# Kernel optimization log

Hardware: AMD Instinct MI355X
Metric: run time of the kernel (lower is better)

Reference implementation:

```python
import jax, jax.numpy as jnp
import numpy as np

N_NODES = 50000
N_EDGES = 800000
IN_C, HID_C, OUT_C = 96, 64, 40
ALPHA = 0.2
K = 2
NEG_SLOPE = 0.01  # F.leaky_relu default


def setup_inputs() -> dict:
    key = jax.random.key(0)
    k_x, k_e, k_w0, k_b0, k_w4, k_b4 = jax.random.split(key, 6)
    x = jax.random.normal(k_x, (N_NODES, IN_C), dtype=jnp.float32)
    edge_index = jax.random.randint(k_e, (2, N_EDGES), 0, N_NODES, dtype=jnp.int64)
    # SGConv linear layers (torch.nn.Linear layout: [out, in])
    W0 = jax.random.normal(k_w0, (HID_C, IN_C), dtype=jnp.float32) / np.sqrt(IN_C)
    b0 = jax.random.normal(k_b0, (HID_C,), dtype=jnp.float32) * 0.01
    W4 = jax.random.normal(k_w4, (OUT_C, HID_C), dtype=jnp.float32) / np.sqrt(HID_C)
    b4 = jax.random.normal(k_b4, (OUT_C,), dtype=jnp.float32) * 0.01
    return {"x": x, "edge_index": edge_index, "W0": W0, "b0": b0, "W4": W4, "b4": b4}


def reference(x, edge_index, W0, b0, W4, b4):
    # GCN normalization with self-loops (shared by SGConv and APPNP in PyG):
    # A_hat = A + I, prop(h) = D^{-1/2} A_hat D^{-1/2} h
    n = x.shape[0]
    loops = jnp.arange(n, dtype=edge_index.dtype)
    src = jnp.concatenate([edge_index[0], loops])
    dst = jnp.concatenate([edge_index[1], loops])
    deg = jax.ops.segment_sum(jnp.ones_like(dst, dtype=x.dtype), dst, num_segments=n)
    dinv = jnp.where(deg > 0, jax.lax.rsqrt(deg), 0.0)
    norm = dinv[src] * dinv[dst]  # [E + N]

    def prop(h):
        # gather -> scale -> scatter-add  (irregular memory-bound core op)
        return jax.ops.segment_sum(norm[:, None] * h[src], dst, num_segments=n)

    def sg_prop(h):  # SGConv: K propagation steps, then linear
        for _ in range(K):
            h = prop(h)
        return h

    def appnp(h0):  # APPNP: z_{k+1} = (1-alpha) * prop(z_k) + alpha * h0
        z = h0
        for _ in range(K):
            z = (1.0 - ALPHA) * prop(z) + ALPHA * h0
        return z

    h = sg_prop(x) @ W0.T + b0          # conv0 (SGConv)
    # dropout is identity in eval mode (training=False)
    h = jax.nn.leaky_relu(appnp(h), NEG_SLOPE)   # conv1
    h = jax.nn.leaky_relu(appnp(h), NEG_SLOPE)   # conv2
    h = jax.nn.leaky_relu(appnp(h), NEG_SLOPE)   # conv3
    h = sg_prop(h) @ W4.T + b4          # conv4 (SGConv)
    return jax.nn.log_softmax(h, axis=1)
```

## Files before the change

### kernel.cpp

```cpp
#include <hip/hip_runtime.h>
#include <hip/hip_fp16.h>
#include <math.h>

#define N_NODES 50000
#define N_EDGES 800000
#define IN_C 96
#define HID_C 64
#define OUT_C 40
#define ALPHA 0.2f
#define NEG_SLOPE 0.01f

typedef _Float16 f16x8 __attribute__((ext_vector_type(8)));
typedef float f32x4 __attribute__((ext_vector_type(4)));

__device__ __forceinline__ int edge_at(const void* ei, int is64, long long pos) {
    return is64 ? (int)((const long long*)ei)[pos] : ((const int*)ei)[pos];
}

__global__ void zero_detect_k(int* deg, int n, const unsigned int* ei, int* flag) {
    int i = blockIdx.x * blockDim.x + threadIdx.x;
    if (i < n) deg[i] = 0;
    if (i == 0) {
        int is64 = 1;
        for (int j = 1; j < 16; j += 2)
            if (ei[j] != 0u) is64 = 0;
        *flag = is64;
    }
}

__global__ void deg_hist_k(const void* ei, const int* flag, int* deg, int E) {
    int e = blockIdx.x * blockDim.x + threadIdx.x;
    if (e < E) {
        int d = edge_at(ei, *flag, (long long)E + e);
        atomicAdd(&deg[d], 1);
    }
}

__global__ void scan_p1_k(const int* __restrict__ deg, int* __restrict__ part, int n) {
    __shared__ int sm[256];
    int t = threadIdx.x, i = blockIdx.x * 256 + t;
    int v = (i < n) ? deg[i] : 0;
    sm[t] = v;
    __syncthreads();
    for (int off = 1; off < 256; off <<= 1) {
        int u = (t >= off) ? sm[t - off] : 0;
        __syncthreads();
        sm[t] += u;
        __syncthreads();
    }
    if (t == 255) part[blockIdx.x] = sm[255];
}

__global__ void scan_p2_k(int* part, int nb, int* rowptr, int n) {
    __shared__ int sm[256];
    int t = threadIdx.x;
    int v = (t < nb) ? part[t] : 0;
    sm[t] = v;
    __syncthreads();
    for (int off = 1; off < 256; off <<= 1) {
        int u = (t >= off) ? sm[t - off] : 0;
        __syncthreads();
        sm[t] += u;
        __syncthreads();
    }
    if (t < nb) part[t] = sm[t] - v;
    if (t == 255) rowptr[n] = sm[255];
}

__global__ void scan_p3_k(const int* __restrict__ deg, const int* __restrict__ part,
                          int* __restrict__ rowptr, int* __restrict__ cursor,
                          float* __restrict__ dinv, int n) {
    __shared__ int sm[256];
    int t = threadIdx.x, i = blockIdx.x * 256 + t;
    int v = (i < n) ? deg[i] : 0;
    sm[t] = v;
    __syncthreads();
    for (int off = 1; off < 256; off <<= 1) {
        int u = (t >= off) ? sm[t - off] : 0;
        __syncthreads();
        sm[t] += u;
        __syncthreads();
    }
    if (i < n) {
        int excl = sm[t] - v + part[blockIdx.x];
        rowptr[i] = excl;
        cursor[i] = excl;
        dinv[i] = rsqrtf((float)v + 1.0f);
    }
}

__global__ void bhist_k(const int* __restrict__ deg, int* __restrict__ bcnt, int n) {
    __shared__ int h[64];
    int t = threadIdx.x, i = blockIdx.x * 256 + t;
    if (t < 64) h[t] = 0;
    __syncthreads();
    if (i < n) {
        int d = deg[i]; if (d > 63) d = 63;
        atomicAdd(&h[63 - d], 1);
    }
    __syncthreads();
    if (t < 64) bcnt[blockIdx.x * 64 + t] = h[t];
}

__global__ void bscanA_k(const int* __restrict__ bcnt, int* __restrict__ bbase,
                         int* __restrict__ tot, int nb) {
    __shared__ int sm[256];
    int b = blockIdx.x;
    int t = threadIdx.x;
    int v = (t < nb) ? bcnt[t * 64 + b] : 0;
    sm[t] = v;
    __syncthreads();
    for (int off = 1; off < 256; off <<= 1) {
        int u = (t >= off) ? sm[t - off] : 0;
        __syncthreads();
        sm[t] += u;
        __syncthreads();
    }
    if (t < nb) bbase[t * 64 + b] = sm[t] - v;
    if (t == 255) tot[b] = sm[255];
}

__global__ void bscanB_k(const int* __restrict__ tot, int* __restrict__ bstart) {
    __shared__ int sm[64];
    int t = threadIdx.x;
    int v = tot[t];
    sm[t] = v;
    __syncthreads();
    for (int off = 1; off < 64; off <<= 1) {
        int u = (t >= off) ? sm[t - off] : 0;
        __syncthreads();
        sm[t] += u;
        __syncthreads();
    }
    bstart[t] = sm[t] - v;
}

__global__ void perm_k(const int* __restrict__ deg, const int* __restrict__ bbase,
                       const int* __restrict__ bstart, int* __restrict__ perm, int n) {
    __shared__ int h[64];
    int t = threadIdx.x, i = blockIdx.x * 256 + t;
    if (t < 64) h[t] = 0;
    __syncthreads();
    if (i < n) {
        int d = deg[i]; if (d > 63) d = 63;
        int b = 63 - d;
        int rank = atomicAdd(&h[b], 1);
        perm[bstart[b] + bbase[blockIdx.x * 64 + b] + rank] = i;
    }
}

#define FILL_CHUNK 2048
__global__ void csr_fill_k(const void* ei, const int* flag,
                           int* __restrict__ cursor, int* __restrict__ csrc,
                           int E, int N) {
    int p = blockIdx.x & 7;
    int chunk = blockIdx.x >> 3;
    int lo = p * (N / 8), hi = lo + (N / 8);
    int e0 = chunk * FILL_CHUNK;
    int e1 = e0 + FILL_CHUNK; if (e1 > E) e1 = E;
    int f = *flag;
    for (int e = e0 + threadIdx.x; e < e1; e += 2 * blockDim.x) {
        int e2 = e + blockDim.x;
        int d0 = edge_at(ei, f, (long long)E + e);
        int d1 = (e2 < e1) ? edge_at(ei, f, (long long)E + e2) : -1;
        if (d0 >= lo && d0 < hi) {
            int s = edge_at(ei, f, e);
            int pos = atomicAdd(&cursor[d0], 1);
            csrc[pos] = s;
        }
        if (d1 >= lo && d1 < hi) {
            int s = edge_at(ei, f, e2);
            int pos = atomicAdd(&cursor[d1], 1);
            csrc[pos] = s;
        }
    }
}

template <bool COMBINE, bool LEAKY, bool BIAS>
__global__ void prop64_k(const int* __restrict__ perm,
                         const int* __restrict__ rowptr, const int* __restrict__ csrc,
                         const float* __restrict__ dinv,
                         const __half* __restrict__ in, const __half* __restrict__ h0,
                         const float* __restrict__ bias,
                         __half* __restrict__ out, int N) {
    int qw = blockIdx.x * (blockDim.x >> 4) + (threadIdx.x >> 4);
    int ci = threadIdx.x & 15;
    if (qw >= N) return;
    int node = perm[qw];
    const float2* in4 = (const float2*)in;
    f32x4 acc;
    {
        float2 r = in4[node * 16 + ci];
        float2 a = __half22float2(*(const __half2*)&r.x);
        float2 b = __half22float2(*(const __half2*)&r.y);
        acc[0] = a.x; acc[1] = a.y; acc[2] = b.x; acc[3] = b.y;
    }
    int r0 = rowptr[node], r1 = rowptr[node + 1];
    int i = r0;
    for (; i + 3 < r1; i += 4) {
        int s0 = csrc[i], s1 = csrc[i + 1], s2 = csrc[i + 2], s3 = csrc[i + 3];
        float2 v0 = in4[s0 * 16 + ci];
        float2 v1 = in4[s1 * 16 + ci];
        float2 v2 = in4[s2 * 16 + ci];
        float2 v3 = in4[s3 * 16 + ci];
        float2 a0 = __half22float2(*(const __half2*)&v0.x), b0 = __half22float2(*(const __half2*)&v0.y);
        float2 a1 = __half22float2(*(const __half2*)&v1.x), b1 = __half22float2(*(const __half2*)&v1.y);
        float2 a2 = __half22float2(*(const __half2*)&v2.x), b2 = __half22float2(*(const __half2*)&v2.y);
        float2 a3 = __half22float2(*(const __half2*)&v3.x), b3 = __half22float2(*(const __half2*)&v3.y);
        acc[0] += (a0.x + a1.x) + (a2.x + a3.x);
        acc[1] += (a0.y + a1.y) + (a2.y + a3.y);
        acc[2] += (b0.x + b1.x) + (b2.x + b3.x);
        acc[3] += (b0.y + b1.y) + (b2.y + b3.y);
    }
    for (; i < r1; ++i) {
        float2 v0 = in4[csrc[i] * 16 + ci];
        float2 a0 = __half22float2(*(const __half2*)&v0.x), b0 = __half22float2(*(const __half2*)&v0.y);
        acc[0] += a0.x; acc[1] += a0.y; acc[2] += b0.x; acc[3] += b0.y;
    }
    float di = dinv[node];
    float sc = di * di;
    float4 v;
    v.x = sc * acc[0]; v.y = sc * acc[1]; v.z = sc * acc[2]; v.w = sc * acc[3];
    if (BIAS) {
        const float4 b = ((const float4*)bias)[ci];
        v.x += di * b.x; v.y += di * b.y; v.z += di * b.z; v.w += di * b.w;
    }
    if (COMBINE) {
        float2 r = ((const float2*)h0)[node * 16 + ci];
        float2 a = __half22float2(*(const __half2*)&r.x);
        float2 b = __half22float2(*(const __half2*)&r.y);
        v.x = (1.0f - ALPHA) * v.x + ALPHA * a.x;
        v.y = (1.0f - ALPHA) * v.y + ALPHA * a.y;
        v.z = (1.0f - ALPHA) * v.z + ALPHA * b.x;
        v.w = (1.0f - ALPHA) * v.w + ALPHA * b.y;
    }
    if (LEAKY) {
        v.x = v.x > 0.0f ? v.x : NEG_SLOPE * v.x;
        v.y = v.y > 0.0f ? v.y : NEG_SLOPE * v.y;
        v.z = v.z > 0.0f ? v.z : NEG_SLOPE * v.z;
        v.w = v.w > 0.0f ? v.w : NEG_SLOPE * v.w;
    }
    float2 o;
    *(__half2*)&o.x = __float22half2_rn(make_float2(v.x, v.y));
    *(__half2*)&o.y = __float22half2_rn(make_float2(v.z, v.w));
    ((float2*)out)[node * 16 + ci] = o;
}

__global__ void prop40_k(const int* __restrict__ perm,
                         const int* __restrict__ rowptr, const int* __restrict__ csrc,
                         const float* __restrict__ dinv,
                         const __half* __restrict__ in, __half* __restrict__ out, int N) {
    constexpr int CP = OUT_C / 2;
    int hw = blockIdx.x * (blockDim.x >> 5) + (threadIdx.x >> 5);
    int ci = threadIdx.x & 31;
    if (hw >= N) return;
    int node = perm[hw];
    bool act = ci < CP;
    const __half2* in2 = (const __half2*)in;
    float2 acc = make_float2(0.0f, 0.0f);
    if (act) {
        acc = __half22float2(in2[(long long)node * CP + ci]);
    }
    int r0 = rowptr[node], r1 = rowptr[node + 1];
    int i = r0;
    for (; i + 3 < r1; i += 4) {
        int s0 = csrc[i], s1 = csrc[i + 1], s2 = csrc[i + 2], s3 = csrc[i + 3];
        if (act) {
            float2 v0 = __half22float2(in2[(long long)s0 * CP + ci]);
            float2 v1 = __half22float2(in2[(long long)s1 * CP + ci]);
            float2 v2 = __half22float2(in2[(long long)s2 * CP + ci]);
            float2 v3 = __half22float2(in2[(long long)s3 * CP + ci]);
            acc.x += (v0.x + v1.x) + (v2.x + v3.x);
            acc.y += (v0.y + v1.y) + (v2.y + v3.y);
        }
    }
    for (; i < r1; ++i) {
        int s0 = csrc[i];
        if (act) {
            float2 v0 = __half22float2(in2[(long long)s0 * CP + ci]);
            acc.x += v0.x; acc.y += v0.y;
        }
    }
    if (act) {
        float di = dinv[node];
        float sc = di * di;
        ((__half2*)out)[(long long)node * CP + ci] =
            __float22half2_rn(make_float2(sc * acc.x, sc * acc.y));
    }
}

__global__ void prop40_softmax_k(const int* __restrict__ perm,
                                 const int* __restrict__ rowptr, const int* __restrict__ csrc,
                                 const float* __restrict__ dinv,
                                 const __half* __restrict__ in, const float* __restrict__ bias,
                                 float* __restrict__ out, int N) {
    constexpr int CP = OUT_C / 2;
    int hw = blockIdx.x * (blockDim.x >> 5) + (threadIdx.x >> 5);
    int ci = threadIdx.x & 31;
    if (hw >= N) return;
    int node = perm[hw];
    bool act = ci < CP;
    const __half2* in2 = (const __half2*)in;
    float2 acc = make_float2(0.0f, 0.0f);
    if (act) {
        acc = __half22float2(in2[(long long)node * CP + ci]);
    }
    int r0 = rowptr[node], r1 = rowptr[node + 1];
    int i = r0;
    for (; i + 3 < r1; i += 4) {
        int s0 = csrc[i], s1 = csrc[i + 1], s2 = csrc[i + 2], s3 = csrc[i + 3];
        if (act) {
            float2 v0 = __half22float2(in2[(long long)s0 * CP + ci]);
            float2 v1 = __half22float2(in2[(long long)s1 * CP + ci]);
            float2 v2 = __half22float2(in2[(long long)s2 * CP + ci]);
            float2 v3 = __half22float2(in2[(long long)s3 * CP + ci]);
            acc.x += (v0.x + v1.x) + (v2.x + v3.x);
            acc.y += (v0.y + v1.y) + (v2.y + v3.y);
        }
    }
    for (; i < r1; ++i) {
        int s0 = csrc[i];
        if (act) {
            float2 v0 = __half22float2(in2[(long long)s0 * CP + ci]);
            acc.x += v0.x; acc.y += v0.y;
        }
    }
    float di = dinv[node];
    float2 v = make_float2(-INFINITY, -INFINITY);
    if (act) {
        v.x = di * acc.x + bias[2 * ci];
        v.y = di * acc.y + bias[2 * ci + 1];
    }
    float m = fmaxf(v.x, v.y);
    #pragma unroll
    for (int off = 16; off >= 1; off >>= 1) m = fmaxf(m, __shfl_xor(m, off));
    float e = act ? (expf(v.x - m) + expf(v.y - m)) : 0.0f;
    #pragma unroll
    for (int off = 16; off >= 1; off >>= 1) e += __shfl_xor(e, off);
    float ls = m + logf(e);
    if (act)
        ((float2*)out)[(long long)node * CP + ci] = make_float2(v.x - ls, v.y - ls);
}

template <int O, int K, bool FP32IN, bool SCALE>
__global__ void __launch_bounds__(256) mfma_lin_k(const void* __restrict__ in_,
                                                  const float* __restrict__ W,
                                                  const float* __restrict__ dinv,
                                                  __half* __restrict__ out, int Mtiles) {
    constexpr int P2 = 52;
    __shared__ __half2 wsh[O * P2];
    for (int idx = threadIdx.x; idx < O * (K / 2); idx += 256) {
        int o = idx / (K / 2), kk = idx - o * (K / 2);
        float2 w2 = ((const float2*)W)[o * (K / 2) + kk];
        wsh[o * P2 + kk] = __floats2half2_rn(w2.x, w2.y);
    }
    __syncthreads();
    int wave = (blockIdx.x * 256 + threadIdx.x) >> 6;
    if (wave >= Mtiles) return;
    int lane = threadIdx.x & 63;
    int lm = lane & 15, q = lane >> 4;
    long long m0 = (long long)wave * 16;
    constexpr int NT = (O + 15) / 16;
    f32x4 acc[NT];
    #pragma unroll
    for (int j = 0; j < NT; ++j) acc[j] = (f32x4){0.f, 0.f, 0.f, 0.f};
    const __half* wsp = (const __half*)wsh;
    #pragma unroll
    for (int k0 = 0; k0 < K; k0 += 32) {
        f16x8 a;
        if (FP32IN) {
            const float* xr = (const float*)in_ + (m0 + lm) * K + k0 + q * 8;
            float4 x0 = ((const float4*)xr)[0];
            float4 x1 = ((const float4*)xr)[1];
            a = (f16x8){(_Float16)x0.x, (_Float16)x0.y, (_Float16)x0.z, (_Float16)x0.w,
                        (_Float16)x1.x, (_Float16)x1.y, (_Float16)x1.z, (_Float16)x1.w};
        } else {
            const __half* xr = (const __half*)in_ + (m0 + lm) * K + k0 + q * 8;
            a = *(const f16x8*)xr;
        }
        #pragma unroll
        for (int j = 0; j < NT; ++j) {
            f16x8 b = *(const f16x8*)(wsp + (16 * j + lm) * (2 * P2) + k0 + q * 8);
            acc[j] = __builtin_amdgcn_mfma_f32_16x16x32_f16(a, b, acc[j], 0, 0, 0);
        }
    }
    #pragma unroll
    for (int r = 0; r < 4; ++r) {
        long long m = m0 + q * 4 + r;
        float sc = SCALE ? dinv[m] : 1.0f;
        #pragma unroll
        for (int j = 0; j < NT; ++j) {
            int col = 16 * j + lm;
            if (col < O) out[m * O + col] = __float2half(acc[j][r] * sc);
        }
    }
}

static inline int cdiv(long long a, long long b) { return (int)((a + b - 1) / b); }
static inline size_t align256(size_t x) { return (x + 255) & ~(size_t)255; }

extern "C" void kernel_launch(void* const* d_in, const int* in_sizes, int n_in,
                              void* d_out, int out_size, void* d_ws, size_t ws_size,
                              hipStream_t stream) {
    const float* x  = (const float*)d_in[0];
    const void*  ei = d_in[1];
    const float* W0 = (const float*)d_in[2];
    const float* b0 = (const float*)d_in[3];
    const float* W4 = (const float*)d_in[4];
    const float* b4 = (const float*)d_in[5];
    float* out = (float*)d_out;

    const int N = N_NODES, E = N_EDGES;
    const int NB = cdiv(N, 256);
    char* ws = (char*)d_ws;
    int*    flag   = (int*)ws;     ws += 256;
    int*    deg    = (int*)ws;     ws += align256((size_t)N * 4);
    int*    rowptr = (int*)ws;     ws += align256((size_t)(N + 1) * 4);
    int*    cursor = (int*)ws;     ws += align256((size_t)N * 4);
    int*    part   = (int*)ws;     ws += align256(256 * 4);
    int*    bcnt   = (int*)ws;     ws += align256((size_t)NB * 64 * 4);
    int*    bbase  = (int*)ws;     ws += align256((size_t)NB * 64 * 4);
    int*    tot    = (int*)ws;     ws += align256(64 * 4);
    int*    bstart = (int*)ws;     ws += align256(64 * 4);
    int*    perm   = (int*)ws;     ws += align256((size_t)N * 4);
    float*  dinv   = (float*)ws;   ws += align256((size_t)N * 4);
    int*    csrc   = (int*)ws;     ws += align256((size_t)E * 4);
    __half* bufA   = (__half*)ws;  ws += align256((size_t)N * HID_C * 2);
    __half* bufB   = (__half*)ws;  ws += align256((size_t)N * HID_C * 2);
    __half* bufC   = (__half*)ws;  ws += align256((size_t)N * HID_C * 2);

    const int T = 256;
    const int MT = N / 16;
    const int LB = cdiv(MT, 4);
    const int P64B = cdiv(N, T / 16);
    const int P40B = cdiv(N, T / 32);

    zero_detect_k<<<cdiv(N, T), T, 0, stream>>>(deg, N, (const unsigned int*)ei, flag);
    deg_hist_k<<<cdiv(E, T), T, 0, stream>>>(ei, flag, deg, E);
    scan_p1_k<<<NB, 256, 0, stream>>>(deg, part, N);
    scan_p2_k<<<1, 256, 0, stream>>>(part, NB, rowptr, N);
    scan_p3_k<<<NB, 256, 0, stream>>>(deg, part, rowptr, cursor, dinv, N);
    bhist_k<<<NB, 256, 0, stream>>>(deg, bcnt, N);
    bscanA_k<<<64, 256, 0, stream>>>(bcnt, bbase, tot, NB);
    bscanB_k<<<1, 64, 0, stream>>>(tot, bstart);
    perm_k<<<NB, 256, 0, stream>>>(deg, bbase, bstart, perm, N);
    csr_fill_k<<<cdiv(E, FILL_CHUNK) * 8, T, 0, stream>>>(ei, flag, cursor, csrc, E, N);

    mfma_lin_k<HID_C, IN_C, true, true><<<LB, 256, 0, stream>>>(x, W0, dinv, bufA, MT);
    prop64_k<false, false, false><<<P64B, T, 0, stream>>>(
        perm, rowptr, csrc, dinv, bufA, nullptr, nullptr, bufB, N);
    prop64_k<false, false, true><<<P64B, T, 0, stream>>>(
        perm, rowptr, csrc, dinv, bufB, nullptr, b0, bufC, N);

    for (int r = 0; r < 3; ++r) {
        prop64_k<true, false, false><<<P64B, T, 0, stream>>>(
            perm, rowptr, csrc, dinv, bufC, bufC, nullptr, bufB, N);
        prop64_k<true, true, false><<<P64B, T, 0, stream>>>(
            perm, rowptr, csrc, dinv, bufB, bufC, nullptr, bufC, N);
    }

    mfma_lin_k<OUT_C, HID_C, false, false><<<LB, 256, 0, stream>>>(bufC, W4, dinv, bufA, MT);
    prop40_k<<<P40B, T, 0, stream>>>(perm, rowptr, csrc, dinv, bufA, bufB, N);
    prop40_softmax_k<<<P40B, T, 0, stream>>>(perm, rowptr, csrc, dinv, bufB, b4, out, N);
}
```

Before: 352.6 us.

## Bucket edges by destination partition in one pass and fuse preprocessing kernels

```diff
diff --git a/kernel.cpp b/kernel.cpp
--- a/kernel.cpp
+++ b/kernel.cpp
@@ -9,6 +9,7 @@
 #define OUT_C 40
 #define ALPHA 0.2f
 #define NEG_SLOPE 0.01f
+#define QCAP 131072
 
 typedef _Float16 f16x8 __attribute__((ext_vector_type(8)));
 typedef float f32x4 __attribute__((ext_vector_type(4)));
@@ -17,9 +18,10 @@
     return is64 ? (int)((const long long*)ei)[pos] : ((const int*)ei)[pos];
 }
 
-__global__ void zero_detect_k(int* deg, int n, const unsigned int* ei, int* flag) {
+__global__ void zero_detect_k(int* deg, int n, int* qtail, const unsigned int* ei, int* flag) {
     int i = blockIdx.x * blockDim.x + threadIdx.x;
     if (i < n) deg[i] = 0;
+    if (i < 8) qtail[i] = 0;
     if (i == 0) {
         int is64 = 1;
         for (int j = 1; j < 16; j += 2)
@@ -28,11 +30,49 @@
     }
 }
 
-__global__ void deg_hist_k(const void* ei, const int* flag, int* deg, int E) {
-    int e = blockIdx.x * blockDim.x + threadIdx.x;
-    if (e < E) {
-        int d = edge_at(ei, *flag, (long long)E + e);
-        atomicAdd(&deg[d], 1);
+__global__ void bucketA_k(const void* ei, const int* flag, int* __restrict__ deg,
+                          int* __restrict__ qtail, int2* __restrict__ queue, int E) {
+    __shared__ int cnt[8], qb[8];
+    int f = *flag;
+    int e0 = blockIdx.x * 1024;
+    if (threadIdx.x < 8) cnt[threadIdx.x] = 0;
+    __syncthreads();
+    int s[4], d[4], p[4], r[4];
+    #pragma unroll
+    for (int k = 0; k < 4; ++k) {
+        int e = e0 + threadIdx.x + k * 256;
+        if (e < E) {
+            d[k] = edge_at(ei, f, (long long)E + e);
+            s[k] = edge_at(ei, f, e);
+            atomicAdd(&deg[d[k]], 1);
+            p[k] = d[k] / (N_NODES / 8);
+            if (p[k] > 7) p[k] = 7;
+            r[k] = atomicAdd(&cnt[p[k]], 1);
+        } else p[k] = -1;
+    }
+    __syncthreads();
+    if (threadIdx.x < 8) qb[threadIdx.x] = atomicAdd(&qtail[threadIdx.x], cnt[threadIdx.x]);
+    __syncthreads();
+    #pragma unroll
+    for (int k = 0; k < 4; ++k) {
+        if (p[k] >= 0) {
+            int pos = qb[p[k]] + r[k];
+            if (pos < QCAP) queue[(size_t)p[k] * QCAP + pos] = make_int2(s[k], d[k]);
+        }
+    }
+}
+
+__global__ void bucketB_k(const int* __restrict__ qtail, const int2* __restrict__ queue,
+                          int* __restrict__ cursor, int* __restrict__ csrc) {
+    int p = blockIdx.x & 7;
+    int j = blockIdx.x >> 3;
+    int J = gridDim.x >> 3;
+    int n = qtail[p]; if (n > QCAP) n = QCAP;
+    const int2* q = queue + (size_t)p * QCAP;
+    for (int i = j * blockDim.x + threadIdx.x; i < n; i += J * blockDim.x) {
+        int2 e = q[i];
+        int pos = atomicAdd(&cursor[e.y], 1);
+        csrc[pos] = e.x;
     }
 }
 
@@ -69,9 +109,11 @@
 
 __global__ void scan_p3_k(const int* __restrict__ deg, const int* __restrict__ part,
                           int* __restrict__ rowptr, int* __restrict__ cursor,
-                          float* __restrict__ dinv, int n) {
+                          float* __restrict__ dinv, int* __restrict__ bcnt, int n) {
     __shared__ int sm[256];
+    __shared__ int h[64];
     int t = threadIdx.x, i = blockIdx.x * 256 + t;
+    if (t < 64) h[t] = 0;
     int v = (i < n) ? deg[i] : 0;
     sm[t] = v;
     __syncthreads();
@@ -86,17 +128,8 @@
         rowptr[i] = excl;
         cursor[i] = excl;
         dinv[i] = rsqrtf((float)v + 1.0f);
-    }
-}
-
-__global__ void bhist_k(const int* __restrict__ deg, int* __restrict__ bcnt, int n) {
-    __shared__ int h[64];
-    int t = threadIdx.x, i = blockIdx.x * 256 + t;
-    if (t < 64) h[t] = 0;
-    __syncthreads();
-    if (i < n) {
-        int d = deg[i]; if (d > 63) d = 63;
-        atomicAdd(&h[63 - d], 1);
+        int dd = v; if (dd > 63) dd = 63;
+        atomicAdd(&h[63 - dd], 1);
     }
     __syncthreads();
     if (t < 64) bcnt[blockIdx.x * 64 + t] = h[t];
@@ -120,59 +153,22 @@
     if (t == 255) tot[b] = sm[255];
 }
 
-__global__ void bscanB_k(const int* __restrict__ tot, int* __restrict__ bstart) {
-    __shared__ int sm[64];
-    int t = threadIdx.x;
-    int v = tot[t];
-    sm[t] = v;
-    __syncthreads();
-    for (int off = 1; off < 64; off <<= 1) {
-        int u = (t >= off) ? sm[t - off] : 0;
-        __syncthreads();
-        sm[t] += u;
-        __syncthreads();
-    }
-    bstart[t] = sm[t] - v;
-}
-
 __global__ void perm_k(const int* __restrict__ deg, const int* __restrict__ bbase,
-                       const int* __restrict__ bstart, int* __restrict__ perm, int n) {
-    __shared__ int h[64];
+                       const int* __restrict__ tot, int* __restrict__ perm, int n) {
+    __shared__ int h[64], bs[64];
     int t = threadIdx.x, i = blockIdx.x * 256 + t;
-    if (t < 64) h[t] = 0;
+    if (t < 64) { h[t] = 0; bs[t] = tot[t]; }
+    __syncthreads();
+    if (t == 0) {
+        int run = 0;
+        for (int k = 0; k < 64; ++k) { int v = bs[k]; bs[k] = run; run += v; }
+    }
     __syncthreads();
     if (i < n) {
         int d = deg[i]; if (d > 63) d = 63;
         int b = 63 - d;
         int rank = atomicAdd(&h[b], 1);
-        perm[bstart[b] + bbase[blockIdx.x * 64 + b] + rank] = i;
-    }
-}
-
-#define FILL_CHUNK 2048
-__global__ void csr_fill_k(const void* ei, const int* flag,
-                           int* __restrict__ cursor, int* __restrict__ csrc,
-                           int E, int N) {
-    int p = blockIdx.x & 7;
-    int chunk = blockIdx.x >> 3;
-    int lo = p * (N / 8), hi = lo + (N / 8);
-    int e0 = chunk * FILL_CHUNK;
-    int e1 = e0 + FILL_CHUNK; if (e1 > E) e1 = E;
-    int f = *flag;
-    for (int e = e0 + threadIdx.x; e < e1; e += 2 * blockDim.x) {
-        int e2 = e + blockDim.x;
-        int d0 = edge_at(ei, f, (long long)E + e);
-        int d1 = (e2 < e1) ? edge_at(ei, f, (long long)E + e2) : -1;
-        if (d0 >= lo && d0 < hi) {
-            int s = edge_at(ei, f, e);
-            int pos = atomicAdd(&cursor[d0], 1);
-            csrc[pos] = s;
-        }
-        if (d1 >= lo && d1 < hi) {
-            int s = edge_at(ei, f, e2);
-            int pos = atomicAdd(&cursor[d1], 1);
-            csrc[pos] = s;
-        }
+        perm[bs[b] + bbase[blockIdx.x * 64 + b] + rank] = i;
     }
 }
 
@@ -421,10 +417,11 @@
     int*    bcnt   = (int*)ws;     ws += align256((size_t)NB * 64 * 4);
     int*    bbase  = (int*)ws;     ws += align256((size_t)NB * 64 * 4);
     int*    tot    = (int*)ws;     ws += align256(64 * 4);
-    int*    bstart = (int*)ws;     ws += align256(64 * 4);
+    int*    qtail  = (int*)ws;     ws += align256(8 * 4);
     int*    perm   = (int*)ws;     ws += align256((size_t)N * 4);
     float*  dinv   = (float*)ws;   ws += align256((size_t)N * 4);
     int*    csrc   = (int*)ws;     ws += align256((size_t)E * 4);
+    int2*   queue  = (int2*)ws;    ws += align256((size_t)8 * QCAP * 8);
     __half* bufA   = (__half*)ws;  ws += align256((size_t)N * HID_C * 2);
     __half* bufB   = (__half*)ws;  ws += align256((size_t)N * HID_C * 2);
     __half* bufC   = (__half*)ws;  ws += align256((size_t)N * HID_C * 2);
@@ -435,16 +432,14 @@
     const int P64B = cdiv(N, T / 16);
     const int P40B = cdiv(N, T / 32);
 
-    zero_detect_k<<<cdiv(N, T), T, 0, stream>>>(deg, N, (const unsigned int*)ei, flag);
-    deg_hist_k<<<cdiv(E, T), T, 0, stream>>>(ei, flag, deg, E);
+    zero_detect_k<<<cdiv(N, T), T, 0, stream>>>(deg, N, qtail, (const unsigned int*)ei, flag);
+    bucketA_k<<<cdiv(E, 1024), T, 0, stream>>>(ei, flag, deg, qtail, queue, E);
     scan_p1_k<<<NB, 256, 0, stream>>>(deg, part, N);
     scan_p2_k<<<1, 256, 0, stream>>>(part, NB, rowptr, N);
-    scan_p3_k<<<NB, 256, 0, stream>>>(deg, part, rowptr, cursor, dinv, N);
-    bhist_k<<<NB, 256, 0, stream>>>(deg, bcnt, N);
+    scan_p3_k<<<NB, 256, 0, stream>>>(deg, part, rowptr, cursor, dinv, bcnt, N);
     bscanA_k<<<64, 256, 0, stream>>>(bcnt, bbase, tot, NB);
-    bscanB_k<<<1, 64, 0, stream>>>(tot, bstart);
-    perm_k<<<NB, 256, 0, stream>>>(deg, bbase, bstart, perm, N);
-    csr_fill_k<<<cdiv(E, FILL_CHUNK) * 8, T, 0, stream>>>(ei, flag, cursor, csrc, E, N);
+    perm_k<<<NB, 256, 0, stream>>>(deg, bbase, tot, perm, N);
+    bucketB_k<<<8 * 64, T, 0, stream>>>(qtail, queue, cursor, csrc);
 
     mfma_lin_k<HID_C, IN_C, true, true><<<LB, 256, 0, stream>>>(x, W0, dinv, bufA, MT);
     prop64_k<false, false, false><<<P64B, T, 0, stream>>>(
```

Measured after the change: 350.9 us. Within noise of the previous version (-0.5%).
